# Performance work log

Hardware: AMD Instinct MI355X
Metric: run time of the kernel (lower is better)

The kernel has to match this reference:

```python
import jax, jax.numpy as jnp
import numpy as np

HEADS = 4
DIM_HEAD = 64
DIM = 256
FMAP = 64
SCALE = DIM_HEAD ** -0.5


def setup_inputs() -> dict:
    key = jax.random.key(0)
    k1, k2, k3, k4 = jax.random.split(key, 4)
    inner = HEADS * DIM_HEAD
    fmap = jax.random.normal(k1, (4, DIM, FMAP, FMAP), dtype=jnp.float32)
    # 1x1 conv weight for qkv projection: (3*inner_dim, dim)
    w_qkv = jax.random.normal(k2, (3 * inner, DIM), dtype=jnp.float32) * (DIM ** -0.5)
    # AbsPosEmb parameters, initialized as randn * dim_head**-0.5 (as in BoTNet)
    pos_height = jax.random.normal(k3, (FMAP, DIM_HEAD), dtype=jnp.float32) * SCALE
    pos_width = jax.random.normal(k4, (FMAP, DIM_HEAD), dtype=jnp.float32) * SCALE
    return {"fmap": fmap, "w_qkv": w_qkv, "pos_height": pos_height, "pos_width": pos_width}


def reference(fmap, w_qkv, pos_height, pos_width):
    b, c, h, w = fmap.shape
    hw = h * w
    # 1x1 conv (no bias) == channel matmul
    qkv = jnp.einsum('bchw,oc->bohw', fmap, w_qkv)  # (b, 3*inner, h, w)
    q, k, v = jnp.split(qkv, 3, axis=1)
    # replicate torch .view(b, heads, h*w, -1): raw row-major reshape
    q = q.reshape(b, HEADS, hw, DIM_HEAD) * SCALE
    k = k.reshape(b, HEADS, hw, DIM_HEAD)
    v = v.reshape(b, HEADS, hw, DIM_HEAD)
    sim = jnp.einsum('bhid,bhjd->bhij', q, k)  # (b, heads, hw, hw)
    # absolute positional bias: emb[j] = height[y] + width[x], j = y*w + x
    emb = (pos_height[:, None, :] + pos_width[None, :, :]).reshape(hw, DIM_HEAD)
    sim = sim + jnp.einsum('bhid,jd->bhij', q, emb)
    attn = jax.nn.softmax(sim, axis=-1)
    out = jnp.einsum('bhij,bhjd->bhid', attn, v)  # (b, heads, hw, dim_head)
    # replicate torch .view(b, heads*dim_head, h, w): raw reshape
    return out.reshape(b, HEADS * DIM_HEAD, h, w)
```

## Files before the change

### kernel.cpp

```cpp
#include <hip/hip_runtime.h>


typedef float  f32x4  __attribute__((ext_vector_type(4)));
typedef __bf16 bf16x8 __attribute__((ext_vector_type(8)));
typedef __bf16 bf16x4 __attribute__((ext_vector_type(4)));

__device__ inline float fast_exp2(float x) {
#if __has_builtin(__builtin_amdgcn_exp2f)
  return __builtin_amdgcn_exp2f(x);
#else
  return exp2f(x);
#endif
}

__device__ inline void glds16(const __bf16* g, __bf16* l) {
  __builtin_amdgcn_global_load_lds(
      (const __attribute__((address_space(1))) void*)g,
      (__attribute__((address_space(3))) void*)l, 16, 0, 0);
}

__global__ __launch_bounds__(256) void w_cvt(
    const float* __restrict__ w, __bf16* __restrict__ wb)
{
  int idx = blockIdx.x * 256 + threadIdx.x;
  f32x4 v = ((const f32x4*)w)[idx];
  bf16x4 o; o[0]=(__bf16)v[0]; o[1]=(__bf16)v[1]; o[2]=(__bf16)v[2]; o[3]=(__bf16)v[3];
  ((bf16x4*)wb)[idx] = o;
}

__global__ __launch_bounds__(256) void qkv_proj(
    const float* __restrict__ fmap, const __bf16* __restrict__ wb,
    const float* __restrict__ ph,   const float* __restrict__ pw,
    __bf16* __restrict__ Qw, __bf16* __restrict__ Kw, __bf16* __restrict__ Vw)
{
  constexpr int LS = 264;
  __shared__ __bf16 Bs[32 * LS];
  const int tid  = threadIdx.x;
  const int wv   = tid >> 6;
  const int lane = tid & 63;
  const int quad = lane >> 4, l15 = lane & 15;
  const int n0 = blockIdx.x * 32;
  const int b  = blockIdx.y;

#pragma unroll
  for (int i = 0; i < 2; ++i) {
    int id = tid + i * 256;
    int ng = id & 7;
    int kg = id >> 3;
    const float* base = fmap + ((size_t)b * 256 + 4 * kg) * 4096 + n0 + 4 * ng;
    f32x4 v0 = *(const f32x4*)(base);
    f32x4 v1 = *(const f32x4*)(base + 4096);
    f32x4 v2 = *(const f32x4*)(base + 8192);
    f32x4 v3 = *(const f32x4*)(base + 12288);
#pragma unroll
    for (int j = 0; j < 4; ++j) {
      bf16x4 o; o[0]=(__bf16)v0[j]; o[1]=(__bf16)v1[j]; o[2]=(__bf16)v2[j]; o[3]=(__bf16)v3[j];
      *(bf16x4*)(&Bs[(4 * ng + j) * LS + 4 * kg]) = o;
    }
  }
  __syncthreads();

  for (int mt = 0; mt < 12; ++mt) {
    const int region = mt >> 2;
    const int obase  = (mt & 3) * 64;
    const __bf16* aptr = wb + (size_t)(mt * 64 + 16 * wv + l15) * 256 + 8 * quad;

    f32x4 acc[2] = {};
#pragma unroll
    for (int k0 = 0; k0 < 256; k0 += 32) {
      bf16x8 af = *(const bf16x8*)(aptr + k0);
      bf16x8 b0 = *(const bf16x8*)(&Bs[(l15)      * LS + k0 + 8 * quad]);
      bf16x8 b1 = *(const bf16x8*)(&Bs[(16 + l15) * LS + k0 + 8 * quad]);
      acc[0] = __builtin_amdgcn_mfma_f32_16x16x32_bf16(af, b0, acc[0], 0, 0, 0);
      acc[1] = __builtin_amdgcn_mfma_f32_16x16x32_bf16(af, b1, acc[1], 0, 0, 0);
    }

#pragma unroll
    for (int t = 0; t < 2; ++t) {
#pragma unroll
      for (int rr = 0; rr < 4; ++rr) {
        int oreg = obase + 16 * wv + 4 * quad + rr;
        int s    = n0 + 16 * t + l15;
        float val = acc[t][rr];
        size_t off = ((size_t)(b * 256 + oreg)) * 4096 + s;
        if (region == 0) {
          Qw[off] = (__bf16)(val * 0.18033688f);
        } else if (region == 1) {
          int g = oreg & 63;
          float bias = ph[g * 64 + (s & 63)] + pw[(s >> 6) * 64 + (s & 63)];
          Kw[off] = (__bf16)(val + bias);
        } else {
          Vw[off] = (__bf16)val;
        }
      }
    }
  }
}

__global__ __launch_bounds__(256) void v_transpose(
    const __bf16* __restrict__ Vw, __bf16* __restrict__ Vt)
{
  __shared__ __bf16 T[64 * 72];
  const int tid = threadIdx.x;
  const int j0  = blockIdx.x * 64;
  const int bh  = blockIdx.y;
  const __bf16* src = Vw + (size_t)bh * 262144;
#pragma unroll
  for (int i = 0; i < 2; ++i) {
    int id = tid + i * 256;
    int r = id >> 3, c = (id & 7) * 8;
    *(bf16x8*)(&T[r * 72 + c]) = *(const bf16x8*)(src + (size_t)(j0 + r) * 64 + c);
  }
  __syncthreads();
#pragma unroll
  for (int i = 0; i < 2; ++i) {
    int id = tid + i * 256;
    int d = id >> 3, jc = (id & 7) * 8;
    bf16x8 o;
#pragma unroll
    for (int z = 0; z < 8; ++z) o[z] = T[(jc + z) * 72 + d];
    *(bf16x8*)(Vt + ((size_t)bh * 64 + d) * 4096 + j0 + jc) = o;
  }
}

__global__ __launch_bounds__(256, 2) void flash_attn(
    const __bf16* __restrict__ Qg, const __bf16* __restrict__ Kg,
    const __bf16* __restrict__ Vtg, __bf16* __restrict__ OP0,
    float* __restrict__ lws, float* __restrict__ Og)
{
  __shared__ __bf16 Ks[64 * 64];
  __shared__ __bf16 Vs[64 * 64];
  const int tid  = threadIdx.x;
  const int wv   = tid >> 6;
  const int lane = tid & 63;
  const int quad = lane >> 4, l15 = lane & 15;
  const int bh = blockIdx.y;
  const int z  = blockIdx.z;
  const int iw = blockIdx.x * 256 + 64 * wv;
  const int jbase = z * 2048;
  const __bf16* Qb = Qg  + (size_t)bh * 262144;
  const __bf16* Kb = Kg  + (size_t)bh * 262144;
  const __bf16* Vb = Vtg + (size_t)bh * 262144;

  bf16x8 qf[4][2];
#pragma unroll
  for (int m = 0; m < 4; ++m)
#pragma unroll
    for (int c = 0; c < 2; ++c)
      qf[m][c] = *(const bf16x8*)(Qb + (size_t)(iw + 16 * m + l15) * 64 + 32 * c + 8 * quad);

  const int r0  = tid >> 3;
  const int kch = tid & 7;
  const int xc  = (kch ^ (r0 & 7)) * 8;
  const int pr0a = r0, pr1a = r0 + 32;
  const int pr0 = (pr0a & 0x23) | ((pr0a & 0x0C) << 1) | ((pr0a & 0x10) >> 2);
  const int pr1 = (pr1a & 0x23) | ((pr1a & 0x0C) << 1) | ((pr1a & 0x10) >> 2);
  const __bf16* kp0 = Kb + (size_t)(jbase + pr0) * 64 + xc;
  const __bf16* kp1 = Kb + (size_t)(jbase + pr1) * 64 + xc;
  const __bf16* vp0 = Vb + (size_t)r0 * 4096        + jbase + xc;
  const __bf16* vp1 = Vb + (size_t)(r0 + 32) * 4096 + jbase + xc;
  __bf16* ldsK0 = &Ks[tid * 8];
  __bf16* ldsK1 = &Ks[tid * 8 + 2048];
  __bf16* ldsV0 = &Vs[tid * 8];
  __bf16* ldsV1 = &Vs[tid * 8 + 2048];

  f32x4 acco[4][4] = {};
  f32x4 l4[4] = {};

  const int swz = (l15 & 7);

  for (int it = 0; it < 32; ++it) {
    glds16(kp0, ldsK0); kp0 += 4096;
    glds16(kp1, ldsK1); kp1 += 4096;
    glds16(vp0, ldsV0); vp0 += 64;
    glds16(vp1, ldsV1); vp1 += 64;
    __syncthreads();

    f32x4 sacc[4][4] = {};
#pragma unroll
    for (int c = 0; c < 2; ++c) {
#pragma unroll
      for (int t = 0; t < 4; ++t) {
        bf16x8 ak = *(const bf16x8*)(&Ks[(16 * t + l15) * 64 + (((4 * c + quad) ^ swz) * 8)]);
#pragma unroll
        for (int m = 0; m < 4; ++m)
          sacc[m][t] = __builtin_amdgcn_mfma_f32_16x16x32_bf16(ak, qf[m][c], sacc[m][t], 0, 0, 0);
      }
    }

    bf16x8 pf[4][2];
#pragma unroll
    for (int m = 0; m < 4; ++m) {
#pragma unroll
      for (int t = 0; t < 4; ++t) {
#pragma unroll
        for (int r = 0; r < 4; ++r) {
          float pv = fast_exp2(sacc[m][t][r]);
          sacc[m][t][r] = pv;
          l4[m][r] += pv;
        }
      }
#pragma unroll
      for (int c2 = 0; c2 < 2; ++c2) {
        bf16x8 a;
#pragma unroll
        for (int r = 0; r < 4; ++r) {
          a[r]     = (__bf16)sacc[m][2 * c2][r];
          a[4 + r] = (__bf16)sacc[m][2 * c2 + 1][r];
        }
        pf[m][c2] = a;
      }
    }

#pragma unroll
    for (int c2 = 0; c2 < 2; ++c2) {
#pragma unroll
      for (int t = 0; t < 4; ++t) {
        bf16x8 bv = *(const bf16x8*)(&Vs[(16 * t + l15) * 64 + (((4 * c2 + quad) ^ swz) * 8)]);
#pragma unroll
        for (int m = 0; m < 4; ++m)
          acco[m][t] = __builtin_amdgcn_mfma_f32_16x16x32_bf16(pf[m][c2], bv, acco[m][t], 0, 0, 0);
      }
    }
    __syncthreads();
  }

#pragma unroll
  for (int m = 0; m < 4; ++m) {
    float l = (l4[m][0] + l4[m][1]) + (l4[m][2] + l4[m][3]);
    l += __shfl_xor(l, 16, 64);
    l += __shfl_xor(l, 32, 64);
    if (quad == 0)
      lws[z * 65536 + bh * 4096 + iw + 16 * m + l15] = l;
  }
  if (z == 0) {
    __bf16* Ob = OP0 + (size_t)bh * 262144;
#pragma unroll
    for (int m = 0; m < 4; ++m)
#pragma unroll
      for (int t = 0; t < 4; ++t)
#pragma unroll
        for (int r = 0; r < 4; ++r)
          Ob[(size_t)(iw + 16 * m + 4 * quad + r) * 64 + 16 * t + l15] =
              (__bf16)acco[m][t][r];
  } else {
    float* Ob = Og + (size_t)bh * 262144;
#pragma unroll
    for (int m = 0; m < 4; ++m)
#pragma unroll
      for (int t = 0; t < 4; ++t)
#pragma unroll
        for (int r = 0; r < 4; ++r)
          Ob[(size_t)(iw + 16 * m + 4 * quad + r) * 64 + 16 * t + l15] =
              acco[m][t][r];
  }
}

__global__ __launch_bounds__(256) void combine(
    const __bf16* __restrict__ OP0, const float* __restrict__ lws,
    float* __restrict__ Og)
{
  int idx = blockIdx.x * 256 + threadIdx.x;
  int row = idx >> 4;
  float inv = 1.0f / (lws[row] + lws[65536 + row]);
  f32x4 o = ((const f32x4*)Og)[idx];
  bf16x4 p = ((const bf16x4*)OP0)[idx];
  f32x4 r;
#pragma unroll
  for (int k = 0; k < 4; ++k) r[k] = (o[k] + (float)p[k]) * inv;
  ((f32x4*)Og)[idx] = r;
}

extern "C" void kernel_launch(void* const* d_in, const int* in_sizes, int n_in,
                              void* d_out, int out_size, void* d_ws, size_t ws_size,
                              hipStream_t stream) {
  const float* fmap = (const float*)d_in[0];
  const float* w    = (const float*)d_in[1];
  const float* ph   = (const float*)d_in[2];
  const float* pw   = (const float*)d_in[3];
  float* out = (float*)d_out;

  __bf16* Qw = (__bf16*)d_ws;
  __bf16* Kw = Qw + 4194304;
  __bf16* Vw = Kw + 4194304;
  __bf16* Vt = Vw + 4194304;
  float*  lws = (float*)(Vt + 4194304);
  __bf16* Wb16 = (__bf16*)(lws + 131072);

  w_cvt      <<<dim3(192),       256, 0, stream>>>(w, Wb16);
  qkv_proj   <<<dim3(128, 4),    256, 0, stream>>>(fmap, Wb16, ph, pw, Qw, Kw, Vw);
  v_transpose<<<dim3(64, 16),    256, 0, stream>>>(Vw, Vt);
  flash_attn <<<dim3(16, 16, 2), 256, 0, stream>>>(Qw, Kw, Vt, Vw , lws, out);
  combine    <<<dim3(4096),      256, 0, stream>>>(Vw , lws, out);
}
```

Measured before the change: 185.4 us.

## Double-buffer K/V tiles in LDS to overlap DMA with MFMA compute

Doubles the shared K and V buffers and restructures the flash-attention loop as a two-stage ping-pong. The direct global-to-LDS loads for the next tile are issued before the current tile's QK^T, exp and PV MFMAs run. The aim is to hide global load latency, which the old one-buffer scheme exposed at every barrier. In exchange, LDS use per block doubles to 32 KB, and the loop becomes a manually unrolled two-tile body with one fewer barrier per tile.

```diff
diff --git a/kernel.cpp b/kernel.cpp
--- a/kernel.cpp
+++ b/kernel.cpp
@@ -128,8 +128,8 @@
     const __bf16* __restrict__ Vtg, __bf16* __restrict__ OP0,
     float* __restrict__ lws, float* __restrict__ Og)
 {
-  __shared__ __bf16 Ks[64 * 64];
-  __shared__ __bf16 Vs[64 * 64];
+  __shared__ __bf16 Ks[2 * 64 * 64];
+  __shared__ __bf16 Vs[2 * 64 * 64];
   const int tid  = threadIdx.x;
   const int wv   = tid >> 6;
   const int lane = tid & 63;
@@ -159,35 +159,34 @@
   const __bf16* kp1 = Kb + (size_t)(jbase + pr1) * 64 + xc;
   const __bf16* vp0 = Vb + (size_t)r0 * 4096        + jbase + xc;
   const __bf16* vp1 = Vb + (size_t)(r0 + 32) * 4096 + jbase + xc;
-  __bf16* ldsK0 = &Ks[tid * 8];
-  __bf16* ldsK1 = &Ks[tid * 8 + 2048];
-  __bf16* ldsV0 = &Vs[tid * 8];
-  __bf16* ldsV1 = &Vs[tid * 8 + 2048];
 
   f32x4 acco[4][4] = {};
   f32x4 l4[4] = {};
-
   const int swz = (l15 & 7);
 
-  for (int it = 0; it < 32; ++it) {
-    glds16(kp0, ldsK0); kp0 += 4096;
-    glds16(kp1, ldsK1); kp1 += 4096;
-    glds16(vp0, ldsV0); vp0 += 64;
-    glds16(vp1, ldsV1); vp1 += 64;
-    __syncthreads();
-
+  auto dma_tile = [&](int buf) {
+    __bf16* k0 = &Ks[buf * 4096 + tid * 8];
+    __bf16* v0 = &Vs[buf * 4096 + tid * 8];
+    glds16(kp0, k0);        kp0 += 4096;
+    glds16(kp1, k0 + 2048); kp1 += 4096;
+    glds16(vp0, v0);        vp0 += 64;
+    glds16(vp1, v0 + 2048); vp1 += 64;
+  };
+
+  auto compute_tile = [&](int buf) {
+    const __bf16* Kbuf = &Ks[buf * 4096];
+    const __bf16* Vbuf = &Vs[buf * 4096];
     f32x4 sacc[4][4] = {};
 #pragma unroll
     for (int c = 0; c < 2; ++c) {
 #pragma unroll
       for (int t = 0; t < 4; ++t) {
-        bf16x8 ak = *(const bf16x8*)(&Ks[(16 * t + l15) * 64 + (((4 * c + quad) ^ swz) * 8)]);
+        bf16x8 ak = *(const bf16x8*)(&Kbuf[(16 * t + l15) * 64 + (((4 * c + quad) ^ swz) * 8)]);
 #pragma unroll
         for (int m = 0; m < 4; ++m)
           sacc[m][t] = __builtin_amdgcn_mfma_f32_16x16x32_bf16(ak, qf[m][c], sacc[m][t], 0, 0, 0);
       }
     }
-
     bf16x8 pf[4][2];
 #pragma unroll
     for (int m = 0; m < 4; ++m) {
@@ -211,18 +210,26 @@
         pf[m][c2] = a;
       }
     }
-
 #pragma unroll
     for (int c2 = 0; c2 < 2; ++c2) {
 #pragma unroll
       for (int t = 0; t < 4; ++t) {
-        bf16x8 bv = *(const bf16x8*)(&Vs[(16 * t + l15) * 64 + (((4 * c2 + quad) ^ swz) * 8)]);
+        bf16x8 bv = *(const bf16x8*)(&Vbuf[(16 * t + l15) * 64 + (((4 * c2 + quad) ^ swz) * 8)]);
 #pragma unroll
         for (int m = 0; m < 4; ++m)
           acco[m][t] = __builtin_amdgcn_mfma_f32_16x16x32_bf16(pf[m][c2], bv, acco[m][t], 0, 0, 0);
       }
     }
+  };
+
+  dma_tile(0);
+  for (int it = 0; it < 32; it += 2) {
     __syncthreads();
+    dma_tile(1);
+    compute_tile(0);
+    __syncthreads();
+    if (it < 30) dma_tile(0);
+    compute_tile(1);
   }
 
 #pragma unroll
```

New measurement: 182.0 us. Within noise of the previous version (-1.8%).
